# Kernel tuning notes

Measured on AMD Instinct MI355X. Metric: run time of the kernel, lower is better.

## Reference

```python
import jax, jax.numpy as jnp
import numpy as np

D_MODEL = 768
NUM_HEADS = 12
D_K = D_MODEL // NUM_HEADS
D_FF = 2048
LN_EPS = 1e-3  # Keras LayerNormalization default
B, S = 4, 2048


def layer_norm(x, gamma, beta):
    mu = jnp.mean(x, axis=-1, keepdims=True)
    var = jnp.var(x, axis=-1, keepdims=True)
    return (x - mu) * jax.lax.rsqrt(var + LN_EPS) * gamma + beta


def setup_inputs() -> dict:
    key = jax.random.key(0)
    ks = jax.random.split(key, 16)
    sd = 0.02
    inp = {
        "x": jax.random.normal(ks[0], (B, S, D_MODEL), dtype=jnp.float32),
        "src_mask": jnp.zeros((B, 1, 1, S), dtype=jnp.float32),
        "Wq": jax.random.normal(ks[1], (D_MODEL, D_MODEL), jnp.float32) * sd,
        "bq": jnp.zeros((D_MODEL,), jnp.float32),
        "Wk": jax.random.normal(ks[2], (D_MODEL, D_MODEL), jnp.float32) * sd,
        "bk": jnp.zeros((D_MODEL,), jnp.float32),
        "Wv": jax.random.normal(ks[3], (D_MODEL, D_MODEL), jnp.float32) * sd,
        "bv": jnp.zeros((D_MODEL,), jnp.float32),
        "Wo": jax.random.normal(ks[4], (D_MODEL, D_MODEL), jnp.float32) * sd,
        "bo": jnp.zeros((D_MODEL,), jnp.float32),
        "W1": jax.random.normal(ks[5], (D_MODEL, D_FF), jnp.float32) * sd,
        "b1": jnp.zeros((D_FF,), jnp.float32),
        "W2": jax.random.normal(ks[6], (D_FF, D_MODEL), jnp.float32) * sd,
        "b2": jnp.zeros((D_MODEL,), jnp.float32),
        "gamma1": jnp.ones((D_MODEL,), jnp.float32),
        "beta1": jnp.zeros((D_MODEL,), jnp.float32),
        "gamma2": jnp.ones((D_MODEL,), jnp.float32),
        "beta2": jnp.zeros((D_MODEL,), jnp.float32),
    }
    return inp


def encoder_layer(x, src_mask, Wq, bq, Wk, bk, Wv, bv, Wo, bo, W1, b1, W2, b2,
                  gamma1, beta1, gamma2, beta2):
    b, s, _ = x.shape
    def heads(t):  # [B,S,D] -> [B,H,S,Dk]
        return t.reshape(b, s, NUM_HEADS, D_K).transpose(0, 2, 1, 3)
    Q = heads(x @ Wq + bq)
    K = heads(x @ Wk + bk)
    V = heads(x @ Wv + bv)
    scores = jnp.einsum("bhqd,bhkd->bhqk", Q, K) / jnp.sqrt(jnp.float32(D_K))
    scores = scores + src_mask * (-1e9)
    probs = jax.nn.softmax(scores, axis=-1)
    attn = jnp.einsum("bhqk,bhkd->bhqd", probs, V)
    attn = attn.transpose(0, 2, 1, 3).reshape(b, s, D_MODEL)
    attn_out = attn @ Wo + bo
    # dropout is identity at inference
    x1 = layer_norm(x + attn_out, gamma1, beta1)
    ff = jax.nn.relu(x1 @ W1 + b1) @ W2 + b2
    return layer_norm(x1 + ff, gamma2, beta2)


def reference(x, src_mask, Wq, bq, Wk, bk, Wv, bv, Wo, bo, W1, b1, W2, b2,
              gamma1, beta1, gamma2, beta2):
    return encoder_layer(x, src_mask, Wq, bq, Wk, bk, Wv, bv, Wo, bo,
                         W1, b1, W2, b2, gamma1, beta1, gamma2, beta2)
```

## Files before the change

### kernel.cpp

```cpp
#include <hip/hip_runtime.h>


typedef unsigned short u16;
typedef __bf16 bf16x8 __attribute__((ext_vector_type(8)));
typedef __bf16 bf16x4 __attribute__((ext_vector_type(4)));
typedef unsigned short u16x8 __attribute__((ext_vector_type(8)));
typedef float f32x4 __attribute__((ext_vector_type(4)));

#define D_MODEL 768
#define D_FF    2048
#define NH      12
#define DK      64
#define S_LEN   2048
#define M_TOK   8192

#define QSCALE   0.18033688011112042f
#define MSCALE  -1.4426950408889634e9f

__device__ __forceinline__ float bf2f(u16 v) {
    union { unsigned u; float f; } c; c.u = ((unsigned)v) << 16; return c.f;
}
__device__ __forceinline__ void st_bf(u16* p, float v) { *(__bf16*)p = (__bf16)v; }

__device__ __forceinline__ void gload_lds16(const void* g, void* l) {
    __builtin_amdgcn_global_load_lds(
        (const __attribute__((address_space(1))) void*)g,
        (__attribute__((address_space(3))) void*)l, 16, 0, 0);
}

__global__ __launch_bounds__(256)
void cvt_k(const float* __restrict__ in, u16* __restrict__ out, int n) {
    const int i = (blockIdx.x * 256 + threadIdx.x) * 4;
    const float4 v = *(const float4*)(in + i);
    __bf16 o[4] = {(__bf16)v.x, (__bf16)v.y, (__bf16)v.z, (__bf16)v.w};
    *(bf16x4*)(out + i) = *(bf16x4*)o;
}

__global__ __launch_bounds__(256)
void tr4_k(const float* __restrict__ Wq, const float* __restrict__ Wk,
           const float* __restrict__ Wv, const float* __restrict__ Wo,
           u16* __restrict__ WqkvT, u16* __restrict__ WoT) {
    const int z = blockIdx.z;
    const float* in = z == 0 ? Wq : (z == 1 ? Wk : (z == 2 ? Wv : Wo));
    u16* out = z == 3 ? WoT : WqkvT + z * 768 * 768;
    __shared__ float t[32][33];
    const int tx = threadIdx.x & 31, ty = threadIdx.x >> 5;
    const int bx = blockIdx.x * 32, by = blockIdx.y * 32;
#pragma unroll
    for (int i = 0; i < 32; i += 8)
        t[ty + i][tx] = in[(size_t)(by + ty + i) * 768 + bx + tx];
    __syncthreads();
#pragma unroll
    for (int i = 0; i < 32; i += 8)
        st_bf(&out[(size_t)(bx + ty + i) * 768 + by + tx], t[tx][ty + i]);
}

__global__ __launch_bounds__(256)
void transpose_k(const float* __restrict__ in, u16* __restrict__ out, int R, int C) {
    __shared__ float t[32][33];
    const int tx = threadIdx.x & 31, ty = threadIdx.x >> 5;
    const int bx = blockIdx.x * 32, by = blockIdx.y * 32;
#pragma unroll
    for (int i = 0; i < 32; i += 8)
        t[ty + i][tx] = in[(size_t)(by + ty + i) * C + bx + tx];
    __syncthreads();
#pragma unroll
    for (int i = 0; i < 32; i += 8)
        st_bf(&out[(size_t)(bx + ty + i) * R + by + tx], t[tx][ty + i]);
}

__global__ __launch_bounds__(256, 2)
void qkv_gemm_k(const u16* __restrict__ A, const u16* __restrict__ Bt,
                const float* __restrict__ bq, const float* __restrict__ bk,
                const float* __restrict__ bv, u16* __restrict__ Qb,
                u16* __restrict__ Kb, u16* __restrict__ Vt) {
    __shared__ __align__(16) u16 As[128 * 32];
    __shared__ __align__(16) u16 Bs[128 * 32];
    const int tid = threadIdx.x;
    const int lane = tid & 63, w = tid >> 6;
    const int r16 = lane & 15, qd = lane >> 4;
    const int m0 = blockIdx.x * 128, n0 = blockIdx.y * 128;
    const int wm = (w & 1) << 6, wn = (w >> 1) << 6;
    const int K = D_MODEL;

    f32x4 acc[4][4] = {};

    const u16* aP[2]; const u16* bP[2]; u16* aL[2]; u16* bL[2];
#pragma unroll
    for (int it = 0; it < 2; ++it) {
        const int f = it * 256 + tid;
        const int row = f >> 2, kc = (f & 3) << 3;
        aP[it] = A  + (size_t)(m0 + row) * K + kc;
        bP[it] = Bt + (size_t)(n0 + row) * K + kc;
        aL[it] = &As[f * 8];
        bL[it] = &Bs[f * 8];
    }

    for (int k0 = 0; k0 < K; k0 += 32) {
#pragma unroll
        for (int it = 0; it < 2; ++it) {
            gload_lds16(aP[it] + k0, aL[it]);
            gload_lds16(bP[it] + k0, bL[it]);
        }
        __syncthreads();
        bf16x8 af[4], bfr[4];
#pragma unroll
        for (int i = 0; i < 4; ++i) {
            af[i]  = *(const bf16x8*)&As[(wm + i * 16 + r16) * 32 + qd * 8];
            bfr[i] = *(const bf16x8*)&Bs[(wn + i * 16 + r16) * 32 + qd * 8];
        }
#pragma unroll
        for (int i = 0; i < 4; ++i)
#pragma unroll
            for (int j = 0; j < 4; ++j)
                acc[i][j] = __builtin_amdgcn_mfma_f32_16x16x32_bf16(af[i], bfr[j], acc[i][j], 0, 0, 0);
        __syncthreads();
    }

    const int sel = n0 < 768 ? 0 : (n0 < 1536 ? 1 : 2);
    const float* bias = sel == 0 ? bq : (sel == 1 ? bk : bv);
    const float scale = sel == 0 ? QSCALE : 1.0f;
    const int nbase = n0 - sel * 768;

#pragma unroll
    for (int j = 0; j < 4; ++j) {
        const int ncol = nbase + wn + j * 16 + r16;
        const float bvv = bias[ncol];
#pragma unroll
        for (int i = 0; i < 4; ++i) {
#pragma unroll
            for (int rr = 0; rr < 4; ++rr) {
                const int m = m0 + wm + i * 16 + qd * 4 + rr;
                const float v = (acc[i][j][rr] + bvv) * scale;
                if (sel == 0) {
                    st_bf(&Qb[(size_t)m * D_MODEL + ncol], v);
                } else if (sel == 1) {
                    st_bf(&Kb[(size_t)m * D_MODEL + ncol], v);
                } else {
                    const int h = ncol >> 6, d = ncol & 63;
                    const int bb = m >> 11, np = m & 2047;
                    st_bf(&Vt[(((size_t)(bb * NH + h)) * DK + d) * S_LEN + np], v);
                }
            }
        }
    }
}

__global__ __launch_bounds__(256, 2)
void gemm_bt_k(const u16* __restrict__ A, const u16* __restrict__ Bt,
               const float* __restrict__ bias, u16* __restrict__ Cout,
               int M, int N, int K, int mode) {
    __shared__ __align__(16) u16 As[128 * 32];
    __shared__ __align__(16) u16 Bs[128 * 32];
    const int tid = threadIdx.x;
    const int lane = tid & 63, w = tid >> 6;
    const int r16 = lane & 15, qd = lane >> 4;
    const int m0 = blockIdx.x * 128, n0 = blockIdx.y * 128;
    const int wm = (w & 1) << 6, wn = (w >> 1) << 6;

    f32x4 acc[4][4] = {};

    const u16* aP[2]; const u16* bP[2]; u16* aL[2]; u16* bL[2];
#pragma unroll
    for (int it = 0; it < 2; ++it) {
        const int f = it * 256 + tid;
        const int row = f >> 2, kc = (f & 3) << 3;
        aP[it] = A  + (size_t)(m0 + row) * K + kc;
        bP[it] = Bt + (size_t)(n0 + row) * K + kc;
        aL[it] = &As[f * 8];
        bL[it] = &Bs[f * 8];
    }

    for (int k0 = 0; k0 < K; k0 += 32) {
#pragma unroll
        for (int it = 0; it < 2; ++it) {
            gload_lds16(aP[it] + k0, aL[it]);
            gload_lds16(bP[it] + k0, bL[it]);
        }
        __syncthreads();
        bf16x8 af[4], bfr[4];
#pragma unroll
        for (int i = 0; i < 4; ++i) {
            af[i]  = *(const bf16x8*)&As[(wm + i * 16 + r16) * 32 + qd * 8];
            bfr[i] = *(const bf16x8*)&Bs[(wn + i * 16 + r16) * 32 + qd * 8];
        }
#pragma unroll
        for (int i = 0; i < 4; ++i)
#pragma unroll
            for (int j = 0; j < 4; ++j)
                acc[i][j] = __builtin_amdgcn_mfma_f32_16x16x32_bf16(af[i], bfr[j], acc[i][j], 0, 0, 0);
        __syncthreads();
    }

#pragma unroll
    for (int j = 0; j < 4; ++j) {
        const int n = n0 + wn + j * 16 + r16;
        const float bv = bias ? bias[n] : 0.0f;
#pragma unroll
        for (int i = 0; i < 4; ++i) {
#pragma unroll
            for (int rr = 0; rr < 4; ++rr) {
                const int m = m0 + wm + i * 16 + qd * 4 + rr;
                float v = acc[i][j][rr] + bv;
                if (mode == 2) v = fmaxf(v, 0.0f);
                st_bf(&Cout[(size_t)m * N + n], v);
            }
        }
    }
}

__global__ __launch_bounds__(256, 3)
void gemm_bt64_k(const u16* __restrict__ A, const u16* __restrict__ Bt,
                 const float* __restrict__ bias, u16* __restrict__ Cout,
                 int M, int N, int K, int mode) {
    __shared__ __align__(16) u16 As[64 * 32];
    __shared__ __align__(16) u16 Bs[128 * 32];
    const int tid = threadIdx.x;
    const int lane = tid & 63, w = tid >> 6;
    const int r16 = lane & 15, qd = lane >> 4;
    const int m0 = blockIdx.x * 64, n0 = blockIdx.y * 128;
    const int wm = (w & 1) << 5, wn = (w >> 1) << 6;

    f32x4 acc[2][4] = {};

    const int arow = tid >> 2, akc = (tid & 3) << 3;
    const u16* aP = A + (size_t)(m0 + arow) * K + akc;
    u16* aL = &As[tid * 8];
    const u16* bP[2]; u16* bL[2];
#pragma unroll
    for (int it = 0; it < 2; ++it) {
        const int f = it * 256 + tid;
        const int row = f >> 2, kc = (f & 3) << 3;
        bP[it] = Bt + (size_t)(n0 + row) * K + kc;
        bL[it] = &Bs[f * 8];
    }

    for (int k0 = 0; k0 < K; k0 += 32) {
        gload_lds16(aP + k0, aL);
#pragma unroll
        for (int it = 0; it < 2; ++it)
            gload_lds16(bP[it] + k0, bL[it]);
        __syncthreads();
        bf16x8 af[2], bfr[4];
#pragma unroll
        for (int i = 0; i < 2; ++i)
            af[i] = *(const bf16x8*)&As[(wm + i * 16 + r16) * 32 + qd * 8];
#pragma unroll
        for (int j = 0; j < 4; ++j)
            bfr[j] = *(const bf16x8*)&Bs[(wn + j * 16 + r16) * 32 + qd * 8];
#pragma unroll
        for (int i = 0; i < 2; ++i)
#pragma unroll
            for (int j = 0; j < 4; ++j)
                acc[i][j] = __builtin_amdgcn_mfma_f32_16x16x32_bf16(af[i], bfr[j], acc[i][j], 0, 0, 0);
        __syncthreads();
    }

#pragma unroll
    for (int j = 0; j < 4; ++j) {
        const int n = n0 + wn + j * 16 + r16;
        const float bv = bias ? bias[n] : 0.0f;
#pragma unroll
        for (int i = 0; i < 2; ++i) {
#pragma unroll
            for (int rr = 0; rr < 4; ++rr) {
                const int m = m0 + wm + i * 16 + qd * 4 + rr;
                float v = acc[i][j][rr] + bv;
                if (mode == 2) v = fmaxf(v, 0.0f);
                st_bf(&Cout[(size_t)m * N + n], v);
            }
        }
    }
}

#define TS 72

__global__ __launch_bounds__(256, 3)
void attn_k(const u16* __restrict__ Qg, const u16* __restrict__ Kg,
            const u16* __restrict__ Vtg, const float* __restrict__ maskg,
            u16* __restrict__ Og) {
    const int tid = threadIdx.x, lane = tid & 63, w = tid >> 6;
    const int r16 = lane & 15, qd = lane >> 4;
    const int q0 = blockIdx.x * 128;
    const int h = blockIdx.y, b = blockIdx.z;

    __shared__ __align__(16) u16 Ks[64 * TS];
    __shared__ __align__(16) u16 Vts[64 * TS];
    __shared__ __align__(16) u16 Ps[128 * TS];

    bf16x8 qa[2][2];
#pragma unroll
    for (int mt = 0; mt < 2; ++mt)
#pragma unroll
        for (int ks = 0; ks < 2; ++ks)
            qa[mt][ks] = *(const bf16x8*)(Qg +
                ((size_t)((b * S_LEN + q0 + w * 32 + mt * 16 + r16) * NH + h)) * DK +
                ks * 32 + qd * 8);

    const int srow = tid >> 3, sc = (tid & 7) << 3;
    u16x8 kreg[2], vreg[2];
#pragma unroll
    for (int it = 0; it < 2; ++it) {
        const int row = srow + it * 32;
        kreg[it] = *(const u16x8*)(Kg + ((size_t)((b * S_LEN + row) * NH + h)) * DK + sc);
        vreg[it] = *(const u16x8*)(Vtg + (((size_t)(b * NH + h)) * DK + row) * S_LEN + sc);
    }

    float l_i[2] = {0.0f, 0.0f};
    f32x4 Oacc[2][4] = {};

    for (int kt = 0; kt < S_LEN / 64; ++kt) {
        const int ks0 = kt * 64;

#pragma unroll
        for (int it = 0; it < 2; ++it) {
            const int row = srow + it * 32;
            *(u16x8*)&Ks[row * TS + sc]  = kreg[it];
            *(u16x8*)&Vts[row * TS + sc] = vreg[it];
        }
        __syncthreads();

        if (kt + 1 < S_LEN / 64) {
            const int ns0 = ks0 + 64;
#pragma unroll
            for (int it = 0; it < 2; ++it) {
                const int row = srow + it * 32;
                kreg[it] = *(const u16x8*)(Kg + ((size_t)((b * S_LEN + ns0 + row) * NH + h)) * DK + sc);
                vreg[it] = *(const u16x8*)(Vtg + (((size_t)(b * NH + h)) * DK + row) * S_LEN + ns0 + sc);
            }
        }

        f32x4 sa[2][4] = {};
#pragma unroll
        for (int ks = 0; ks < 2; ++ks) {
            bf16x8 kb[4];
#pragma unroll
            for (int nt = 0; nt < 4; ++nt)
                kb[nt] = *(const bf16x8*)&Ks[(nt * 16 + r16) * TS + ks * 32 + qd * 8];
#pragma unroll
            for (int mt = 0; mt < 2; ++mt)
#pragma unroll
                for (int nt = 0; nt < 4; ++nt)
                    sa[mt][nt] = __builtin_amdgcn_mfma_f32_16x16x32_bf16(kb[nt], qa[mt][ks], sa[mt][nt], 0, 0, 0);
        }

        float4 mrow[4];
#pragma unroll
        for (int nt = 0; nt < 4; ++nt) {
            const float4 mm = ((const float4*)(maskg + (size_t)b * S_LEN + ks0))[nt * 4 + qd];
            mrow[nt].x = mm.x * MSCALE; mrow[nt].y = mm.y * MSCALE;
            mrow[nt].z = mm.z * MSCALE; mrow[nt].w = mm.w * MSCALE;
        }

#pragma unroll
        for (int mt = 0; mt < 2; ++mt) {
            float rsum = 0.0f;
#pragma unroll
            for (int nt = 0; nt < 4; ++nt) {
                sa[mt][nt][0] = __builtin_amdgcn_exp2f(sa[mt][nt][0] + mrow[nt].x);
                sa[mt][nt][1] = __builtin_amdgcn_exp2f(sa[mt][nt][1] + mrow[nt].y);
                sa[mt][nt][2] = __builtin_amdgcn_exp2f(sa[mt][nt][2] + mrow[nt].z);
                sa[mt][nt][3] = __builtin_amdgcn_exp2f(sa[mt][nt][3] + mrow[nt].w);
                rsum += sa[mt][nt][0] + sa[mt][nt][1] + sa[mt][nt][2] + sa[mt][nt][3];
            }
            rsum += __shfl_xor(rsum, 16);
            rsum += __shfl_xor(rsum, 32);
            l_i[mt] += rsum;
        }

#pragma unroll
        for (int mt = 0; mt < 2; ++mt)
#pragma unroll
            for (int nt = 0; nt < 4; ++nt) {
                __bf16 pk[4];
#pragma unroll
                for (int rr = 0; rr < 4; ++rr) pk[rr] = (__bf16)sa[mt][nt][rr];
                *(bf16x4*)&Ps[(w * 32 + mt * 16 + r16) * TS + nt * 16 + qd * 4] = *(bf16x4*)pk;
            }

#pragma unroll
        for (int ks = 0; ks < 2; ++ks) {
            bf16x8 pa[2], vb[4];
#pragma unroll
            for (int mt = 0; mt < 2; ++mt)
                pa[mt] = *(const bf16x8*)&Ps[(w * 32 + mt * 16 + r16) * TS + ks * 32 + qd * 8];
#pragma unroll
            for (int vt = 0; vt < 4; ++vt)
                vb[vt] = *(const bf16x8*)&Vts[(vt * 16 + r16) * TS + ks * 32 + qd * 8];
#pragma unroll
            for (int mt = 0; mt < 2; ++mt)
#pragma unroll
                for (int vt = 0; vt < 4; ++vt)
                    Oacc[mt][vt] = __builtin_amdgcn_mfma_f32_16x16x32_bf16(pa[mt], vb[vt], Oacc[mt][vt], 0, 0, 0);
        }
        __syncthreads();
    }

#pragma unroll
    for (int mt = 0; mt < 2; ++mt) {
        const float linv = 1.0f / l_i[mt];
#pragma unroll
        for (int rr = 0; rr < 4; ++rr) {
            const float lr = __shfl(linv, qd * 4 + rr);
            const int qrow = q0 + w * 32 + mt * 16 + qd * 4 + rr;
#pragma unroll
            for (int vt = 0; vt < 4; ++vt)
                st_bf(&Og[((size_t)((b * S_LEN + qrow) * NH + h)) * DK + vt * 16 + r16],
                      Oacc[mt][vt][rr] * lr);
        }
    }
}

__global__ __launch_bounds__(256, 4)
void resln_k(const u16* __restrict__ xb, const u16* __restrict__ yb,
             const float* __restrict__ gamma, const float* __restrict__ beta,
             u16* __restrict__ outb, float* __restrict__ outf) {
    const int row = blockIdx.x, tid = threadIdx.x;
    const int lane = tid & 63, w = tid >> 6;
    __shared__ float redS[4], redS2[4];
    const size_t base = (size_t)row * D_MODEL;
    float h[3], s = 0.0f, s2 = 0.0f;
#pragma unroll
    for (int i = 0; i < 3; ++i) {
        const int c = i * 256 + tid;
        const float v = bf2f(xb[base + c]) + bf2f(yb[base + c]);
        h[i] = v; s += v; s2 += v * v;
    }
#pragma unroll
    for (int off = 32; off >= 1; off >>= 1) { s += __shfl_xor(s, off); s2 += __shfl_xor(s2, off); }
    if (lane == 0) { redS[w] = s; redS2[w] = s2; }
    __syncthreads();
    s  = redS[0] + redS[1] + redS[2] + redS[3];
    s2 = redS2[0] + redS2[1] + redS2[2] + redS2[3];
    const float mu  = s * (1.0f / D_MODEL);
    const float var = s2 * (1.0f / D_MODEL) - mu * mu;
    const float rstd = rsqrtf(var + 1e-3f);
#pragma unroll
    for (int i = 0; i < 3; ++i) {
        const int c = i * 256 + tid;
        const float o = (h[i] - mu) * rstd * gamma[c] + beta[c];
        if (outb) st_bf(&outb[base + c], o);
        if (outf) outf[base + c] = o;
    }
}

extern "C" void kernel_launch(void* const* d_in, const int* in_sizes, int n_in,
                              void* d_out, int out_size, void* d_ws, size_t ws_size,
                              hipStream_t stream) {
    (void)in_sizes; (void)n_in; (void)out_size; (void)ws_size;
    const float* x    = (const float*)d_in[0];
    const float* mask = (const float*)d_in[1];
    const float* Wq = (const float*)d_in[2];  const float* bq  = (const float*)d_in[3];
    const float* Wk = (const float*)d_in[4];  const float* bk  = (const float*)d_in[5];
    const float* Wv = (const float*)d_in[6];  const float* bv  = (const float*)d_in[7];
    const float* Wo = (const float*)d_in[8];  const float* bo  = (const float*)d_in[9];
    const float* W1 = (const float*)d_in[10]; const float* b1  = (const float*)d_in[11];
    const float* W2 = (const float*)d_in[12]; const float* b2  = (const float*)d_in[13];
    const float* g1 = (const float*)d_in[14]; const float* be1 = (const float*)d_in[15];
    const float* g2 = (const float*)d_in[16]; const float* be2 = (const float*)d_in[17];

    char* ws = (char*)d_ws;
    u16* xb     = (u16*)(ws + 0);
    u16* WqkvT  = (u16*)(ws + 12582912);
    u16* WoT    = (u16*)(ws + 16121856);
    u16* W1T    = (u16*)(ws + 17301504);
    u16* W2T    = (u16*)(ws + 20447232);
    u16* Qb     = (u16*)(ws + 23592960);
    u16* Kb     = (u16*)(ws + 36175872);
    u16* Vtg    = (u16*)(ws + 48758784);
    u16* Ab     = (u16*)(ws + 61341696);
    u16* Yb     = (u16*)(ws + 73924608);
    u16* X1b    = (u16*)(ws + 86507520);
    u16* H1b    = (u16*)(ws + 23592960);
    u16* Y2b    = (u16*)(ws + 73924608);

    const dim3 blk(256);

    cvt_k<<<dim3(M_TOK * D_MODEL / 1024), blk, 0, stream>>>(x, xb, M_TOK * D_MODEL);

    tr4_k<<<dim3(24, 24, 4), blk, 0, stream>>>(Wq, Wk, Wv, Wo, WqkvT, WoT);
    transpose_k<<<dim3(64, 24), blk, 0, stream>>>(W1, W1T, D_MODEL, D_FF);
    transpose_k<<<dim3(24, 64), blk, 0, stream>>>(W2, W2T, D_FF, D_MODEL);

    qkv_gemm_k<<<dim3(64, 18), blk, 0, stream>>>(xb, WqkvT, bq, bk, bv, Qb, Kb, Vtg);

    attn_k<<<dim3(16, NH, 4), blk, 0, stream>>>(Qb, Kb, Vtg, mask, Ab);

    gemm_bt64_k<<<dim3(128, 6), blk, 0, stream>>>(Ab, WoT, bo, Yb, M_TOK, D_MODEL, D_MODEL, 1);

    resln_k<<<dim3(M_TOK), blk, 0, stream>>>(xb, Yb, g1, be1, X1b, nullptr);

    gemm_bt_k<<<dim3(64, 16), blk, 0, stream>>>(X1b, W1T, b1, H1b, M_TOK, D_FF, D_MODEL, 2);

    gemm_bt64_k<<<dim3(128, 6), blk, 0, stream>>>(H1b, W2T, b2, Y2b, M_TOK, D_MODEL, D_FF, 1);

    resln_k<<<dim3(M_TOK), blk, 0, stream>>>(X1b, Y2b, g2, be2, nullptr, (float*)d_out);
}
```

Before: 380.0 us.

## Merge prep kernels, deepen GEMM K-step, vectorize V stores, fold mask into accumulator

Replaces the four launches for input conversion and weight transposes with one prep kernel that picks its work by block index. All three GEMM kernels now stage 64-wide K chunks as two 32-wide LDS buffers per barrier, halving the number of barriers per tile. The QKV epilogue writes the transposed V with 4-wide vector stores. The attention kernel loads the mask earlier and seeds the score accumulator with it, which removes the separate add before exp2. Together these cut launch count, synchronization and store instructions, at the cost of doubled LDS use per GEMM block.

```diff
diff --git a/kernel.cpp b/kernel.cpp
--- a/kernel.cpp
+++ b/kernel.cpp
@@ -29,37 +29,37 @@
 }
 
 __global__ __launch_bounds__(256)
-void cvt_k(const float* __restrict__ in, u16* __restrict__ out, int n) {
-    const int i = (blockIdx.x * 256 + threadIdx.x) * 4;
-    const float4 v = *(const float4*)(in + i);
-    __bf16 o[4] = {(__bf16)v.x, (__bf16)v.y, (__bf16)v.z, (__bf16)v.w};
-    *(bf16x4*)(out + i) = *(bf16x4*)o;
-}
-
-__global__ __launch_bounds__(256)
-void tr4_k(const float* __restrict__ Wq, const float* __restrict__ Wk,
-           const float* __restrict__ Wv, const float* __restrict__ Wo,
-           u16* __restrict__ WqkvT, u16* __restrict__ WoT) {
-    const int z = blockIdx.z;
-    const float* in = z == 0 ? Wq : (z == 1 ? Wk : (z == 2 ? Wv : Wo));
-    u16* out = z == 3 ? WoT : WqkvT + z * 768 * 768;
+void prep_k(const float* __restrict__ x, const float* __restrict__ Wq,
+            const float* __restrict__ Wk, const float* __restrict__ Wv,
+            const float* __restrict__ Wo, const float* __restrict__ W1,
+            const float* __restrict__ W2, u16* __restrict__ xb,
+            u16* __restrict__ WqkvT, u16* __restrict__ WoT,
+            u16* __restrict__ W1T, u16* __restrict__ W2T) {
     __shared__ float t[32][33];
-    const int tx = threadIdx.x & 31, ty = threadIdx.x >> 5;
-    const int bx = blockIdx.x * 32, by = blockIdx.y * 32;
-#pragma unroll
-    for (int i = 0; i < 32; i += 8)
-        t[ty + i][tx] = in[(size_t)(by + ty + i) * 768 + bx + tx];
-    __syncthreads();
-#pragma unroll
-    for (int i = 0; i < 32; i += 8)
-        st_bf(&out[(size_t)(bx + ty + i) * 768 + by + tx], t[tx][ty + i]);
-}
-
-__global__ __launch_bounds__(256)
-void transpose_k(const float* __restrict__ in, u16* __restrict__ out, int R, int C) {
-    __shared__ float t[32][33];
-    const int tx = threadIdx.x & 31, ty = threadIdx.x >> 5;
-    const int bx = blockIdx.x * 32, by = blockIdx.y * 32;
+    const int id = blockIdx.x, tid = threadIdx.x;
+    if (id >= 5376) {
+        const int i = ((id - 5376) * 256 + tid) * 4;
+        const float4 v = *(const float4*)(x + i);
+        __bf16 o[4] = {(__bf16)v.x, (__bf16)v.y, (__bf16)v.z, (__bf16)v.w};
+        *(bf16x4*)(xb + i) = *(bf16x4*)o;
+        return;
+    }
+    const float* in; u16* out; int R, C, bx, by;
+    if (id < 2304) {
+        const int z = id / 576, r = id % 576;
+        in = z == 0 ? Wq : (z == 1 ? Wk : (z == 2 ? Wv : Wo));
+        out = z == 3 ? WoT : WqkvT + z * 768 * 768;
+        R = 768; C = 768; bx = (r % 24) * 32; by = (r / 24) * 32;
+    } else if (id < 3840) {
+        const int r = id - 2304;
+        in = W1; out = W1T; R = 768; C = 2048;
+        bx = (r % 64) * 32; by = (r / 64) * 32;
+    } else {
+        const int r = id - 3840;
+        in = W2; out = W2T; R = 2048; C = 768;
+        bx = (r % 24) * 32; by = (r / 24) * 32;
+    }
+    const int tx = tid & 31, ty = tid >> 5;
 #pragma unroll
     for (int i = 0; i < 32; i += 8)
         t[ty + i][tx] = in[(size_t)(by + ty + i) * C + bx + tx];
@@ -74,8 +74,8 @@
                 const float* __restrict__ bq, const float* __restrict__ bk,
                 const float* __restrict__ bv, u16* __restrict__ Qb,
                 u16* __restrict__ Kb, u16* __restrict__ Vt) {
-    __shared__ __align__(16) u16 As[128 * 32];
-    __shared__ __align__(16) u16 Bs[128 * 32];
+    __shared__ __align__(16) u16 As[2][128 * 32];
+    __shared__ __align__(16) u16 Bs[2][128 * 32];
     const int tid = threadIdx.x;
     const int lane = tid & 63, w = tid >> 6;
     const int r16 = lane & 15, qd = lane >> 4;
@@ -85,35 +85,39 @@
 
     f32x4 acc[4][4] = {};
 
-    const u16* aP[2]; const u16* bP[2]; u16* aL[2]; u16* bL[2];
+    const u16* aP[2]; const u16* bP[2]; int f8[2];
 #pragma unroll
     for (int it = 0; it < 2; ++it) {
         const int f = it * 256 + tid;
         const int row = f >> 2, kc = (f & 3) << 3;
         aP[it] = A  + (size_t)(m0 + row) * K + kc;
         bP[it] = Bt + (size_t)(n0 + row) * K + kc;
-        aL[it] = &As[f * 8];
-        bL[it] = &Bs[f * 8];
-    }
-
-    for (int k0 = 0; k0 < K; k0 += 32) {
-#pragma unroll
-        for (int it = 0; it < 2; ++it) {
-            gload_lds16(aP[it] + k0, aL[it]);
-            gload_lds16(bP[it] + k0, bL[it]);
-        }
-        __syncthreads();
-        bf16x8 af[4], bfr[4];
-#pragma unroll
-        for (int i = 0; i < 4; ++i) {
-            af[i]  = *(const bf16x8*)&As[(wm + i * 16 + r16) * 32 + qd * 8];
-            bfr[i] = *(const bf16x8*)&Bs[(wn + i * 16 + r16) * 32 + qd * 8];
-        }
-#pragma unroll
-        for (int i = 0; i < 4; ++i)
-#pragma unroll
-            for (int j = 0; j < 4; ++j)
-                acc[i][j] = __builtin_amdgcn_mfma_f32_16x16x32_bf16(af[i], bfr[j], acc[i][j], 0, 0, 0);
+        f8[it] = f * 8;
+    }
+
+    for (int k0 = 0; k0 < K; k0 += 64) {
+#pragma unroll
+        for (int p = 0; p < 2; ++p)
+#pragma unroll
+            for (int it = 0; it < 2; ++it) {
+                gload_lds16(aP[it] + k0 + p * 32, &As[p][f8[it]]);
+                gload_lds16(bP[it] + k0 + p * 32, &Bs[p][f8[it]]);
+            }
+        __syncthreads();
+#pragma unroll
+        for (int p = 0; p < 2; ++p) {
+            bf16x8 af[4], bfr[4];
+#pragma unroll
+            for (int i = 0; i < 4; ++i) {
+                af[i]  = *(const bf16x8*)&As[p][(wm + i * 16 + r16) * 32 + qd * 8];
+                bfr[i] = *(const bf16x8*)&Bs[p][(wn + i * 16 + r16) * 32 + qd * 8];
+            }
+#pragma unroll
+            for (int i = 0; i < 4; ++i)
+#pragma unroll
+                for (int j = 0; j < 4; ++j)
+                    acc[i][j] = __builtin_amdgcn_mfma_f32_16x16x32_bf16(af[i], bfr[j], acc[i][j], 0, 0, 0);
+        }
         __syncthreads();
     }
 
@@ -128,18 +132,21 @@
         const float bvv = bias[ncol];
 #pragma unroll
         for (int i = 0; i < 4; ++i) {
-#pragma unroll
-            for (int rr = 0; rr < 4; ++rr) {
-                const int m = m0 + wm + i * 16 + qd * 4 + rr;
-                const float v = (acc[i][j][rr] + bvv) * scale;
-                if (sel == 0) {
-                    st_bf(&Qb[(size_t)m * D_MODEL + ncol], v);
-                } else if (sel == 1) {
-                    st_bf(&Kb[(size_t)m * D_MODEL + ncol], v);
-                } else {
-                    const int h = ncol >> 6, d = ncol & 63;
-                    const int bb = m >> 11, np = m & 2047;
-                    st_bf(&Vt[(((size_t)(bb * NH + h)) * DK + d) * S_LEN + np], v);
+            if (sel == 2) {
+                const int h = ncol >> 6, d = ncol & 63;
+                const int mb = m0 + wm + i * 16 + qd * 4;
+                const int bb = mb >> 11, npb = mb & 2047;
+                __bf16 pk[4];
+#pragma unroll
+                for (int rr = 0; rr < 4; ++rr) pk[rr] = (__bf16)(acc[i][j][rr] + bvv);
+                *(bf16x4*)&Vt[(((size_t)(bb * NH + h)) * DK + d) * S_LEN + npb] = *(bf16x4*)pk;
+            } else {
+#pragma unroll
+                for (int rr = 0; rr < 4; ++rr) {
+                    const int m = m0 + wm + i * 16 + qd * 4 + rr;
+                    const float v = (acc[i][j][rr] + bvv) * scale;
+                    if (sel == 0) st_bf(&Qb[(size_t)m * D_MODEL + ncol], v);
+                    else          st_bf(&Kb[(size_t)m * D_MODEL + ncol], v);
                 }
             }
         }
@@ -150,8 +157,8 @@
 void gemm_bt_k(const u16* __restrict__ A, const u16* __restrict__ Bt,
                const float* __restrict__ bias, u16* __restrict__ Cout,
                int M, int N, int K, int mode) {
-    __shared__ __align__(16) u16 As[128 * 32];
-    __shared__ __align__(16) u16 Bs[128 * 32];
+    __shared__ __align__(16) u16 As[2][128 * 32];
+    __shared__ __align__(16) u16 Bs[2][128 * 32];
     const int tid = threadIdx.x;
     const int lane = tid & 63, w = tid >> 6;
     const int r16 = lane & 15, qd = lane >> 4;
@@ -160,35 +167,39 @@
 
     f32x4 acc[4][4] = {};
 
-    const u16* aP[2]; const u16* bP[2]; u16* aL[2]; u16* bL[2];
+    const u16* aP[2]; const u16* bP[2]; int f8[2];
 #pragma unroll
     for (int it = 0; it < 2; ++it) {
         const int f = it * 256 + tid;
         const int row = f >> 2, kc = (f & 3) << 3;
         aP[it] = A  + (size_t)(m0 + row) * K + kc;
         bP[it] = Bt + (size_t)(n0 + row) * K + kc;
-        aL[it] = &As[f * 8];
-        bL[it] = &Bs[f * 8];
-    }
-
-    for (int k0 = 0; k0 < K; k0 += 32) {
-#pragma unroll
-        for (int it = 0; it < 2; ++it) {
-            gload_lds16(aP[it] + k0, aL[it]);
-            gload_lds16(bP[it] + k0, bL[it]);
-        }
-        __syncthreads();
-        bf16x8 af[4], bfr[4];
-#pragma unroll
-        for (int i = 0; i < 4; ++i) {
-            af[i]  = *(const bf16x8*)&As[(wm + i * 16 + r16) * 32 + qd * 8];
-            bfr[i] = *(const bf16x8*)&Bs[(wn + i * 16 + r16) * 32 + qd * 8];
-        }
-#pragma unroll
-        for (int i = 0; i < 4; ++i)
-#pragma unroll
-            for (int j = 0; j < 4; ++j)
-                acc[i][j] = __builtin_amdgcn_mfma_f32_16x16x32_bf16(af[i], bfr[j], acc[i][j], 0, 0, 0);
+        f8[it] = f * 8;
+    }
+
+    for (int k0 = 0; k0 < K; k0 += 64) {
+#pragma unroll
+        for (int p = 0; p < 2; ++p)
+#pragma unroll
+            for (int it = 0; it < 2; ++it) {
+                gload_lds16(aP[it] + k0 + p * 32, &As[p][f8[it]]);
+                gload_lds16(bP[it] + k0 + p * 32, &Bs[p][f8[it]]);
+            }
+        __syncthreads();
+#pragma unroll
+        for (int p = 0; p < 2; ++p) {
+            bf16x8 af[4], bfr[4];
+#pragma unroll
+            for (int i = 0; i < 4; ++i) {
+                af[i]  = *(const bf16x8*)&As[p][(wm + i * 16 + r16) * 32 + qd * 8];
+                bfr[i] = *(const bf16x8*)&Bs[p][(wn + i * 16 + r16) * 32 + qd * 8];
+            }
+#pragma unroll
+            for (int i = 0; i < 4; ++i)
+#pragma unroll
+                for (int j = 0; j < 4; ++j)
+                    acc[i][j] = __builtin_amdgcn_mfma_f32_16x16x32_bf16(af[i], bfr[j], acc[i][j], 0, 0, 0);
+        }
         __syncthreads();
     }
 
@@ -213,8 +224,8 @@
 void gemm_bt64_k(const u16* __restrict__ A, const u16* __restrict__ Bt,
                  const float* __restrict__ bias, u16* __restrict__ Cout,
                  int M, int N, int K, int mode) {
-    __shared__ __align__(16) u16 As[64 * 32];
-    __shared__ __align__(16) u16 Bs[128 * 32];
+    __shared__ __align__(16) u16 As[2][64 * 32];
+    __shared__ __align__(16) u16 Bs[2][128 * 32];
     const int tid = threadIdx.x;
     const int lane = tid & 63, w = tid >> 6;
     const int r16 = lane & 15, qd = lane >> 4;
@@ -225,34 +236,39 @@
 
     const int arow = tid >> 2, akc = (tid & 3) << 3;
     const u16* aP = A + (size_t)(m0 + arow) * K + akc;
-    u16* aL = &As[tid * 8];
-    const u16* bP[2]; u16* bL[2];
+    const u16* bP[2]; int f8[2];
 #pragma unroll
     for (int it = 0; it < 2; ++it) {
         const int f = it * 256 + tid;
         const int row = f >> 2, kc = (f & 3) << 3;
         bP[it] = Bt + (size_t)(n0 + row) * K + kc;
-        bL[it] = &Bs[f * 8];
-    }
-
-    for (int k0 = 0; k0 < K; k0 += 32) {
-        gload_lds16(aP + k0, aL);
-#pragma unroll
-        for (int it = 0; it < 2; ++it)
-            gload_lds16(bP[it] + k0, bL[it]);
-        __syncthreads();
-        bf16x8 af[2], bfr[4];
-#pragma unroll
-        for (int i = 0; i < 2; ++i)
-            af[i] = *(const bf16x8*)&As[(wm + i * 16 + r16) * 32 + qd * 8];
-#pragma unroll
-        for (int j = 0; j < 4; ++j)
-            bfr[j] = *(const bf16x8*)&Bs[(wn + j * 16 + r16) * 32 + qd * 8];
-#pragma unroll
-        for (int i = 0; i < 2; ++i)
+        f8[it] = f * 8;
+    }
+
+    for (int k0 = 0; k0 < K; k0 += 64) {
+#pragma unroll
+        for (int p = 0; p < 2; ++p) {
+            gload_lds16(aP + k0 + p * 32, &As[p][tid * 8]);
+#pragma unroll
+            for (int it = 0; it < 2; ++it)
+                gload_lds16(bP[it] + k0 + p * 32, &Bs[p][f8[it]]);
+        }
+        __syncthreads();
+#pragma unroll
+        for (int p = 0; p < 2; ++p) {
+            bf16x8 af[2], bfr[4];
+#pragma unroll
+            for (int i = 0; i < 2; ++i)
+                af[i] = *(const bf16x8*)&As[p][(wm + i * 16 + r16) * 32 + qd * 8];
 #pragma unroll
             for (int j = 0; j < 4; ++j)
-                acc[i][j] = __builtin_amdgcn_mfma_f32_16x16x32_bf16(af[i], bfr[j], acc[i][j], 0, 0, 0);
+                bfr[j] = *(const bf16x8*)&Bs[p][(wn + j * 16 + r16) * 32 + qd * 8];
+#pragma unroll
+            for (int i = 0; i < 2; ++i)
+#pragma unroll
+                for (int j = 0; j < 4; ++j)
+                    acc[i][j] = __builtin_amdgcn_mfma_f32_16x16x32_bf16(af[i], bfr[j], acc[i][j], 0, 0, 0);
+        }
         __syncthreads();
     }
 
@@ -318,6 +334,14 @@
             *(u16x8*)&Ks[row * TS + sc]  = kreg[it];
             *(u16x8*)&Vts[row * TS + sc] = vreg[it];
         }
+
+        float4 mrow[4];
+#pragma unroll
+        for (int nt = 0; nt < 4; ++nt) {
+            const float4 mm = ((const float4*)(maskg + (size_t)b * S_LEN + ks0))[nt * 4 + qd];
+            mrow[nt].x = mm.x * MSCALE; mrow[nt].y = mm.y * MSCALE;
+            mrow[nt].z = mm.z * MSCALE; mrow[nt].w = mm.w * MSCALE;
+        }
         __syncthreads();
 
         if (kt + 1 < S_LEN / 64) {
@@ -330,7 +354,14 @@
             }
         }
 
-        f32x4 sa[2][4] = {};
+        f32x4 sa[2][4];
+#pragma unroll
+        for (int mt = 0; mt < 2; ++mt)
+#pragma unroll
+            for (int nt = 0; nt < 4; ++nt) {
+                sa[mt][nt][0] = mrow[nt].x; sa[mt][nt][1] = mrow[nt].y;
+                sa[mt][nt][2] = mrow[nt].z; sa[mt][nt][3] = mrow[nt].w;
+            }
 #pragma unroll
         for (int ks = 0; ks < 2; ++ks) {
             bf16x8 kb[4];
@@ -344,23 +375,15 @@
                     sa[mt][nt] = __builtin_amdgcn_mfma_f32_16x16x32_bf16(kb[nt], qa[mt][ks], sa[mt][nt], 0, 0, 0);
         }
 
-        float4 mrow[4];
-#pragma unroll
-        for (int nt = 0; nt < 4; ++nt) {
-            const float4 mm = ((const float4*)(maskg + (size_t)b * S_LEN + ks0))[nt * 4 + qd];
-            mrow[nt].x = mm.x * MSCALE; mrow[nt].y = mm.y * MSCALE;
-            mrow[nt].z = mm.z * MSCALE; mrow[nt].w = mm.w * MSCALE;
-        }
-
 #pragma unroll
         for (int mt = 0; mt < 2; ++mt) {
             float rsum = 0.0f;
 #pragma unroll
             for (int nt = 0; nt < 4; ++nt) {
-                sa[mt][nt][0] = __builtin_amdgcn_exp2f(sa[mt][nt][0] + mrow[nt].x);
-                sa[mt][nt][1] = __builtin_amdgcn_exp2f(sa[mt][nt][1] + mrow[nt].y);
-                sa[mt][nt][2] = __builtin_amdgcn_exp2f(sa[mt][nt][2] + mrow[nt].z);
-                sa[mt][nt][3] = __builtin_amdgcn_exp2f(sa[mt][nt][3] + mrow[nt].w);
+                sa[mt][nt][0] = __builtin_amdgcn_exp2f(sa[mt][nt][0]);
+                sa[mt][nt][1] = __builtin_amdgcn_exp2f(sa[mt][nt][1]);
+                sa[mt][nt][2] = __builtin_amdgcn_exp2f(sa[mt][nt][2]);
+                sa[mt][nt][3] = __builtin_amdgcn_exp2f(sa[mt][nt][3]);
                 rsum += sa[mt][nt][0] + sa[mt][nt][1] + sa[mt][nt][2] + sa[mt][nt][3];
             }
             rsum += __shfl_xor(rsum, 16);
@@ -476,11 +499,8 @@
 
     const dim3 blk(256);
 
-    cvt_k<<<dim3(M_TOK * D_MODEL / 1024), blk, 0, stream>>>(x, xb, M_TOK * D_MODEL);
-
-    tr4_k<<<dim3(24, 24, 4), blk, 0, stream>>>(Wq, Wk, Wv, Wo, WqkvT, WoT);
-    transpose_k<<<dim3(64, 24), blk, 0, stream>>>(W1, W1T, D_MODEL, D_FF);
-    transpose_k<<<dim3(24, 64), blk, 0, stream>>>(W2, W2T, D_FF, D_MODEL);
+    prep_k<<<dim3(11520), blk, 0, stream>>>(x, Wq, Wk, Wv, Wo, W1, W2,
+                                            xb, WqkvT, WoT, W1T, W2T);
 
     qkv_gemm_k<<<dim3(64, 18), blk, 0, stream>>>(xb, WqkvT, bq, bk, bv, Qb, Kb, Vtg);
 
```

Result: faster. 348.1 us (-8.4%).
